# Kernel tuning notes

Measured on AMD Instinct MI355X. Metric: run time of the kernel, lower is better.

The kernel has to match this reference:

```python
import jax, jax.numpy as jnp
import numpy as np

HEADS = 8

def setup_inputs() -> dict:
    key = jax.random.key(0)
    ks = jax.random.split(key, 7)
    B, N, M, C = 4, 2048, 2048, 512
    s = 0.02
    return {
        "hidden_states": jax.random.normal(ks[0], (B, N, C), jnp.float32),
        "encoder_states": jax.random.normal(ks[1], (B, M, C), jnp.float32),
        "Wq": jax.random.normal(ks[2], (C, C), jnp.float32) * s,
        "Wk": jax.random.normal(ks[3], (C, C), jnp.float32) * s,
        "Wv": jax.random.normal(ks[4], (C, C), jnp.float32) * s,
        "Wo": jax.random.normal(ks[5], (C, C), jnp.float32) * s,
        "bo": jnp.zeros((C,), jnp.float32),
    }

def reference(hidden_states, encoder_states, Wq, Wk, Wv, Wo, bo):
    B, N, C = hidden_states.shape
    M = encoder_states.shape[1]
    H = HEADS
    dh = C // H
    scale = dh ** -0.5  # q.shape[-1] ** -0.5 in FlashAttentionFunction / attn.scale
    # projections (to_q/to_k/to_v, no bias as in diffusers CrossAttention)
    q = (hidden_states @ Wq).reshape(B, N, H, dh).transpose(0, 2, 1, 3)   # [B,H,N,dh]
    k = (encoder_states @ Wk).reshape(B, M, H, dh).transpose(0, 2, 1, 3)  # [B,H,M,dh]
    v = (encoder_states @ Wv).reshape(B, M, H, dh).transpose(0, 2, 1, 3)  # [B,H,M,dh]
    # baddbmm(scores) -> softmax -> bmm(values); no mask, non-causal
    scores = jnp.einsum('bhnd,bhmd->bhnm', q, k) * scale                  # [B,H,N,M]
    probs = jax.nn.softmax(scores, axis=-1)
    out = jnp.einsum('bhnm,bhmd->bhnd', probs, v)                         # [B,H,N,dh]
    out = out.transpose(0, 2, 1, 3).reshape(B, N, C)                      # batch_to_head_dim
    return out @ Wo + bo                                                  # to_out[0]; to_out[1] is dropout (identity at eval)
```

## Files before the change

### kernel.cpp

```cpp
#include <hip/hip_runtime.h>
#include <stdint.h>
#include <stddef.h>

typedef __bf16 bf16x8 __attribute__((ext_vector_type(8)));
typedef float f32x4 __attribute__((ext_vector_type(4)));
typedef float f32x16 __attribute__((ext_vector_type(16)));
typedef int int4v __attribute__((ext_vector_type(4)));
typedef unsigned short u16;
typedef unsigned int u32;

__device__ __forceinline__ u16 f2bf(float f) {
    union { float f; unsigned u; } x; x.f = f;
    unsigned r = x.u + 0x7fffu + ((x.u >> 16) & 1u);
    return (u16)(r >> 16);
}

__device__ __forceinline__ float fexp2(float x) { return __builtin_amdgcn_exp2f(x); }

__device__ __forceinline__ u32 cvtpk(float lo, float hi) {
    u32 r;
    asm("v_cvt_pk_bf16_f32 %0, %1, %2" : "=v"(r) : "v"(lo), "v"(hi));
    return r;
}

__device__ __forceinline__ void perm32swap(u32& a, u32& b) {
    asm("v_permlane32_swap_b32 %0, %1" : "+v"(a), "+v"(b));
}

__device__ __forceinline__ f32x16 mfma32(bf16x8 a, bf16x8 b, f32x16 c) {
    return __builtin_amdgcn_mfma_f32_32x32x16_bf16(a, b, c, 0, 0, 0);
}

__device__ __forceinline__ void gl16(const void* g, void* l) {
    __builtin_amdgcn_global_load_lds(
        (const __attribute__((address_space(1))) void*)g,
        (__attribute__((address_space(3))) void*)l, 16, 0, 0);
}

__global__ __launch_bounds__(256) void wtrans4(
        const float* __restrict__ Wq, const float* __restrict__ Wk,
        const float* __restrict__ Wv, const float* __restrict__ Wo,
        u16* __restrict__ oq, u16* __restrict__ ok,
        u16* __restrict__ ov, u16* __restrict__ oo) {
    const int z = blockIdx.z;
    const float* W = (z == 0) ? Wq : (z == 1) ? Wk : (z == 2) ? Wv : Wo;
    u16* O = (z == 0) ? oq : (z == 1) ? ok : (z == 2) ? ov : oo;
    int t  = blockIdx.x * 256 + threadIdx.x;
    int g  = t >> 12;
    int k0 = (t >> 9) & 7;
    int n  = t & 511;
    float v[8];
#pragma unroll
    for (int j = 0; j < 8; ++j)
        v[j] = W[(size_t)(k0 * 64 + g * 8 + j) * 512 + n];
    int gs = g ^ (n & 7);
    u16* dst = O + ((size_t)(k0 * 512 + n) * 8 + gs) * 8;
    ushort4 a, b;
    a.x = f2bf(v[0]); a.y = f2bf(v[1]); a.z = f2bf(v[2]); a.w = f2bf(v[3]);
    b.x = f2bf(v[4]); b.y = f2bf(v[5]); b.z = f2bf(v[6]); b.w = f2bf(v[7]);
    *(ushort4*)dst = a;
    *(ushort4*)(dst + 4) = b;
}

__global__ __launch_bounds__(256) void gemm_qkv(
        const float* __restrict__ hidden, const float* __restrict__ enc,
        const u16* __restrict__ wq, const u16* __restrict__ wk, const u16* __restrict__ wv,
        u16* __restrict__ qo, u16* __restrict__ ko, u16* __restrict__ vo) {
    __shared__ __align__(16) u16 As[128 * 64];
    __shared__ __align__(16) u16 Bs[128 * 64];
    const int z = blockIdx.z;
    const float* A = (z == 0) ? hidden : enc;
    const u16* Bp = (z == 0) ? wq : (z == 1) ? wk : wv;
    const int tid = threadIdx.x, lane = tid & 63, wave = tid >> 6;
    const int wr = (wave >> 1) * 64, wc = (wave & 1) * 64;
    const int brow = blockIdx.x * 128, bcol = blockIdx.y * 128;
    const int lrow = lane & 15;
    const int sr = tid >> 3, sc = tid & 7;

    f32x4 acc[4][4] = {};

    for (int k0s = 0; k0s < 8; ++k0s) {
        const u16* bsrc = Bp + ((size_t)(k0s * 512 + bcol) * 64) + (size_t)(wave * 256 + lane) * 8;
#pragma unroll
        for (int i = 0; i < 4; ++i)
            gl16(bsrc + i * 512, (char*)Bs + wave * 4096 + i * 1024);
#pragma unroll
        for (int i = 0; i < 4; ++i) {
            int r = i * 32 + sr;
            const float* src = A + (size_t)(brow + r) * 512 + k0s * 64 + sc * 8;
            float4 f0 = *(const float4*)src, f1 = *(const float4*)(src + 4);
            int4v w;
            w[0] = cvtpk(f0.x, f0.y); w[1] = cvtpk(f0.z, f0.w);
            w[2] = cvtpk(f1.x, f1.y); w[3] = cvtpk(f1.z, f1.w);
            *(int4v*)((char*)As + r * 128 + ((sc ^ (r & 7)) << 4)) = w;
        }
        __syncthreads();
#pragma unroll
        for (int kc = 0; kc < 2; ++kc) {
            const int kg = kc * 4 + (lane >> 4);
            bf16x8 af[4], bfr[4];
#pragma unroll
            for (int m = 0; m < 4; ++m) {
                int r = wr + m * 16 + lrow;
                af[m] = *(const bf16x8*)((char*)As + r * 128 + ((kg ^ (r & 7)) << 4));
            }
#pragma unroll
            for (int n = 0; n < 4; ++n) {
                int r = wc + n * 16 + lrow;
                bfr[n] = *(const bf16x8*)((char*)Bs + r * 128 + ((kg ^ (r & 7)) << 4));
            }
#pragma unroll
            for (int m = 0; m < 4; ++m)
#pragma unroll
                for (int n = 0; n < 4; ++n)
                    acc[m][n] = __builtin_amdgcn_mfma_f32_16x16x32_bf16(af[m], bfr[n], acc[m][n], 0, 0, 0);
        }
        __syncthreads();
    }

#pragma unroll
    for (int m = 0; m < 4; ++m) {
        int gr0 = brow + wr + m * 16 + ((lane >> 4) << 2);
#pragma unroll
        for (int n = 0; n < 4; ++n) {
            int gc = bcol + wc + n * 16 + lrow;
            int hh = gc >> 6, d = gc & 63;
            if (z == 2) {
                int b = gr0 >> 11, mm = gr0 & 2047;
                ushort4 pk;
                pk.x = f2bf(acc[m][n][0]); pk.y = f2bf(acc[m][n][1]);
                pk.z = f2bf(acc[m][n][2]); pk.w = f2bf(acc[m][n][3]);
                *(ushort4*)(vo + ((size_t)(b * 8 + hh) * 64 + d) * 2048 + mm) = pk;
            } else {
                u16* dst = (z == 0) ? qo : ko;
                const float s = (z == 0) ? 0.125f * 1.44269504f : 1.0f;
#pragma unroll
                for (int j = 0; j < 4; ++j) {
                    int gr = gr0 + j;
                    int b = gr >> 11, nn = gr & 2047;
                    dst[((size_t)(b * 8 + hh) * 2048 + nn) * 64 + d] = f2bf(acc[m][n][j] * s);
                }
            }
        }
    }
}

__global__ __launch_bounds__(256) void gemm_out(
        const u16* __restrict__ A, const u16* __restrict__ Bp,
        const float* __restrict__ bias, float* __restrict__ out) {
    __shared__ __align__(16) u16 As[128 * 64];
    __shared__ __align__(16) u16 Bs[64 * 64];
    const int tid = threadIdx.x, lane = tid & 63, wave = tid >> 6;
    const int wr = (wave >> 1) * 64, wc = (wave & 1) * 32;
    const int brow = blockIdx.x * 128, bcol = blockIdx.y * 64;
    const int lrow = lane & 15;
    const int ar = wave * 32 + (lane >> 3), ag = lane & 7;

    f32x4 acc[4][2] = {};

    for (int k0s = 0; k0s < 8; ++k0s) {
        const u16* asrc = A + (size_t)(brow + ar) * 512 + k0s * 64 + ag * 8;
#pragma unroll
        for (int i = 0; i < 4; ++i)
            gl16(asrc + (size_t)(i * 8) * 512, (char*)As + wave * 4096 + i * 1024);
        const u16* bsrc = Bp + ((size_t)(k0s * 512 + bcol) * 64) + (size_t)(wave * 128 + lane) * 8;
#pragma unroll
        for (int i = 0; i < 2; ++i)
            gl16(bsrc + i * 512, (char*)Bs + wave * 2048 + i * 1024);
        __syncthreads();
#pragma unroll
        for (int kc = 0; kc < 2; ++kc) {
            const int kg = kc * 4 + (lane >> 4);
            bf16x8 af[4], bfr[2];
#pragma unroll
            for (int m = 0; m < 4; ++m) {
                int r = wr + m * 16 + lrow;
                af[m] = *(const bf16x8*)((char*)As + r * 128 + ((kg ^ (r & 7)) << 4));
            }
#pragma unroll
            for (int n = 0; n < 2; ++n) {
                int r = wc + n * 16 + lrow;
                bfr[n] = *(const bf16x8*)((char*)Bs + r * 128 + ((kg ^ (r & 7)) << 4));
            }
#pragma unroll
            for (int m = 0; m < 4; ++m)
#pragma unroll
                for (int n = 0; n < 2; ++n)
                    acc[m][n] = __builtin_amdgcn_mfma_f32_16x16x32_bf16(af[m], bfr[n], acc[m][n], 0, 0, 0);
        }
        __syncthreads();
    }

#pragma unroll
    for (int m = 0; m < 4; ++m) {
        int gr0 = brow + wr + m * 16 + ((lane >> 4) << 2);
#pragma unroll
        for (int n = 0; n < 2; ++n) {
            int gc = bcol + wc + n * 16 + lrow;
            float bv = bias[gc];
#pragma unroll
            for (int j = 0; j < 4; ++j)
                out[(size_t)(gr0 + j) * 512 + gc] = acc[m][n][j] + bv;
        }
    }
}

__global__ __launch_bounds__(1024, 4) void flash_attn(
        const u16* __restrict__ Q, const u16* __restrict__ K,
        const u16* __restrict__ VT, u16* __restrict__ Oa) {
    __shared__ __align__(16) char smem[65536];

    const int tid  = threadIdx.x;
    const int lane = tid & 63;
    const int wave = tid >> 6;
    const int qgrp = wave >> 2;
    const int qtr  = wave & 3;
    const int ql   = lane & 31;
    const int hl   = lane >> 5;
    const int bid  = blockIdx.x;
    const int lid  = (bid & 7) * 64 + (bid >> 3);
    const int bh   = lid >> 4;
    const int qt   = lid & 15;
    const int qg   = qt * 128 + qgrp * 32 + ql;

    const u16* qp = Q + ((size_t)bh * 2048 + qg) * 64 + 8 * hl;
    bf16x8 qf[4];
#pragma unroll
    for (int kc = 0; kc < 4; ++kc) qf[kc] = *(const bf16x8*)(qp + 16 * kc);

    const bool isK = wave < 8;
    const int sq   = isK ? (wave >> 1) : ((wave - 8) >> 1);
    const int i0   = (wave & 1) * 2;
    const int loK = (lane >> 3) * 64 + (((lane & 7) ^ ((lane >> 3) & 7)) * 8);
    const int loV = (lane >> 2) * 2048 + (((lane & 3) ^ ((lane >> 3) & 3)) * 8);
    const u16* gsrc0 = isK
        ? K  + ((size_t)bh * 2048 + sq * 512 + i0 * 8) * 64 + loK
        : VT + (size_t)bh * 131072 + (size_t)(i0 * 16) * 2048 + sq * 512 + loV;
    char* ldst0 = smem + (isK ? 0 : 16384) + sq * 4096 + i0 * 1024;

#define STAGE(b, t) do { \
    const u16* s0_ = gsrc0 + (isK ? (size_t)(t) * 2048 : (size_t)(t) * 32); \
    char* d0_ = ldst0 + (b) * 32768; \
    gl16(s0_, d0_); \
    gl16(s0_ + (isK ? 512 : 32768), d0_ + 1024); \
} while (0)

    f32x16 acc0 = {}, acc1 = {};
    float ls0 = 0.f, ls1 = 0.f, ls2 = 0.f, ls3 = 0.f;

    STAGE(0, 0);
    __syncthreads();

    for (int t = 0; t < 16; ++t) {
        const int b = t & 1;
        if (t < 15) STAGE(b ^ 1, t + 1);

        const char* Kt = smem + b * 32768 + qtr * 4096;
        const char* Vt = smem + b * 32768 + 16384 + qtr * 4096;

        f32x16 st = {};
        __builtin_amdgcn_s_setprio(1);
#pragma unroll
        for (int kc = 0; kc < 4; ++kc) {
            bf16x8 kf = *(const bf16x8*)(Kt + ql * 128 + (((kc * 2 + hl) ^ (ql & 7)) << 4));
            st = mfma32(kf, qf[kc], st);
        }
        __builtin_amdgcn_s_setprio(0);

#pragma unroll
        for (int r = 0; r < 16; r += 4) {
            st[r]   = fexp2(st[r]);   ls0 += st[r];
            st[r+1] = fexp2(st[r+1]); ls1 += st[r+1];
            st[r+2] = fexp2(st[r+2]); ls2 += st[r+2];
            st[r+3] = fexp2(st[r+3]); ls3 += st[r+3];
        }

        __builtin_amdgcn_s_setprio(1);
#pragma unroll
        for (int kc = 0; kc < 2; ++kc) {
            u32 P0 = cvtpk(st[8 * kc + 0], st[8 * kc + 1]);
            u32 P1 = cvtpk(st[8 * kc + 2], st[8 * kc + 3]);
            u32 Q0 = cvtpk(st[8 * kc + 4], st[8 * kc + 5]);
            u32 Q1 = cvtpk(st[8 * kc + 6], st[8 * kc + 7]);
            perm32swap(P0, Q0);
            perm32swap(P1, Q1);
            union { bf16x8 v; u32 u[4]; } bb;
            bb.u[0] = P0; bb.u[1] = P1; bb.u[2] = Q0; bb.u[3] = Q1;
            const int sg = ((kc * 2 + hl) ^ ((ql >> 1) & 3)) << 4;
            bf16x8 v0 = *(const bf16x8*)(Vt + ql * 64 + sg);
            bf16x8 v1 = *(const bf16x8*)(Vt + (32 + ql) * 64 + sg);
            acc0 = mfma32(v0, bb.v, acc0);
            acc1 = mfma32(v1, bb.v, acc1);
        }
        __builtin_amdgcn_s_setprio(0);

        __syncthreads();
    }
#undef STAGE

    float lsum = (ls0 + ls1) + (ls2 + ls3);
    lsum += __shfl_xor(lsum, 32);

    float* CB = (float*)smem;
    float* LS = (float*)(smem + 32768);
    for (int p = 1; p < 4; ++p) {
        if (qtr == p) {
            float* R = CB + qgrp * 2048;
#pragma unroll
            for (int j = 0; j < 4; ++j)
                *(f32x4*)(R + lane * 32 + ((j ^ (lane & 7)) << 2)) =
                    f32x4{acc0[4*j], acc0[4*j+1], acc0[4*j+2], acc0[4*j+3]};
#pragma unroll
            for (int j = 0; j < 4; ++j)
                *(f32x4*)(R + lane * 32 + (((j + 4) ^ (lane & 7)) << 2)) =
                    f32x4{acc1[4*j], acc1[4*j+1], acc1[4*j+2], acc1[4*j+3]};
            LS[qgrp * 64 + lane] = lsum;
        }
        __syncthreads();
        if (qtr == 0) {
            float* R = CB + qgrp * 2048;
#pragma unroll
            for (int j = 0; j < 4; ++j) {
                f32x4 v = *(const f32x4*)(R + lane * 32 + ((j ^ (lane & 7)) << 2));
                acc0[4*j] += v[0]; acc0[4*j+1] += v[1]; acc0[4*j+2] += v[2]; acc0[4*j+3] += v[3];
            }
#pragma unroll
            for (int j = 0; j < 4; ++j) {
                f32x4 v = *(const f32x4*)(R + lane * 32 + (((j + 4) ^ (lane & 7)) << 2));
                acc1[4*j] += v[0]; acc1[4*j+1] += v[1]; acc1[4*j+2] += v[2]; acc1[4*j+3] += v[3];
            }
            lsum += LS[qgrp * 64 + lane];
        }
        __syncthreads();
    }

    if (qtr == 0) {
        float inv = 1.0f / lsum;
        int b_ = bh >> 3, hd = bh & 7;
        u16* orow = Oa + ((size_t)b_ * 2048 + qg) * 512 + hd * 64;
#pragma unroll
        for (int db = 0; db < 2; ++db) {
            const f32x16 a = db ? acc1 : acc0;
#pragma unroll
            for (int rg = 0; rg < 4; ++rg) {
                int d0 = (((db * 4 + rg) ^ (qg & 7)) << 3) + hl * 4;
                ushort4 pk;
                pk.x = f2bf(a[rg * 4 + 0] * inv);
                pk.y = f2bf(a[rg * 4 + 1] * inv);
                pk.z = f2bf(a[rg * 4 + 2] * inv);
                pk.w = f2bf(a[rg * 4 + 3] * inv);
                *(ushort4*)(orow + d0) = pk;
            }
        }
    }
}

extern "C" void kernel_launch(void* const* d_in, const int* in_sizes, int n_in,
                              void* d_out, int out_size, void* d_ws, size_t ws_size,
                              hipStream_t stream) {
    const float* hidden = (const float*)d_in[0];
    const float* enc    = (const float*)d_in[1];
    const float* Wq     = (const float*)d_in[2];
    const float* Wk     = (const float*)d_in[3];
    const float* Wv     = (const float*)d_in[4];
    const float* Wo     = (const float*)d_in[5];
    const float* bo     = (const float*)d_in[6];
    float* out = (float*)d_out;

    char* ws = (char*)d_ws;
    const size_t MB = 1ull << 20;
    u16* q_bf  = (u16*)(ws + 0 * MB);
    u16* k_bf  = (u16*)(ws + 8 * MB);
    u16* vt_bf = (u16*)(ws + 16 * MB);
    u16* at_bf = (u16*)(ws + 24 * MB);
    u16* wq_t  = (u16*)(ws + 32 * MB);
    u16* wk_t  = (u16*)(ws + 32 * MB + 512 * 1024);
    u16* wv_t  = (u16*)(ws + 33 * MB);
    u16* wo_t  = (u16*)(ws + 33 * MB + 512 * 1024);

    dim3 wg(128, 1, 4);
    wtrans4<<<wg, 256, 0, stream>>>(Wq, Wk, Wv, Wo, wq_t, wk_t, wv_t, wo_t);

    dim3 qkvg(64, 4, 3);
    gemm_qkv<<<qkvg, 256, 0, stream>>>(hidden, enc, wq_t, wk_t, wv_t, q_bf, k_bf, vt_bf);

    flash_attn<<<512, 1024, 0, stream>>>(q_bf, k_bf, vt_bf, at_bf);

    dim3 og(64, 8);
    gemm_out<<<og, 256, 0, stream>>>(at_bf, wo_t, bo, out);
}
```

Measured before the change: 95.34 us.

## Pre-swizzle K/V into MFMA fragment layout and load directly from global to registers

The QKV projection now writes K and V in the exact per-lane MFMA fragment order. This lets the attention kernel load them straight from global memory into registers, with double-buffered register prefetch, instead of staging them through LDS with barriers every tile. The attention block shrinks from 1024 to 256 threads. Each wave now handles two 32-row query groups and half of the key range, and the two halves are combined through LDS at the end. This removes LDS traffic and per-tile barriers, at the cost of more registers and no LDS sharing of K/V between waves, so the same data is fetched more times from global memory or L2.

```diff
diff --git a/kernel.cpp b/kernel.cpp
--- a/kernel.cpp
+++ b/kernel.cpp
@@ -124,22 +124,35 @@
 #pragma unroll
         for (int n = 0; n < 4; ++n) {
             int gc = bcol + wc + n * 16 + lrow;
-            int hh = gc >> 6, d = gc & 63;
-            if (z == 2) {
-                int b = gr0 >> 11, mm = gr0 & 2047;
+            int hh2 = gc >> 6, d = gc & 63;
+            int b = gr0 >> 11;
+            int bh2 = b * 8 + hh2;
+            if (z == 0) {
+                int nn = gr0 & 2047;
+#pragma unroll
+                for (int j = 0; j < 4; ++j)
+                    qo[((size_t)bh2 * 2048 + nn + j) * 64 + d] =
+                        f2bf(acc[m][n][j] * (0.125f * 1.44269504f));
+            } else if (z == 1) {
+                int kc = d >> 4, e = d & 7, dl = (d >> 3) & 1;
+#pragma unroll
+                for (int j = 0; j < 4; ++j) {
+                    int nn = (gr0 & 2047) + j;
+                    size_t off = ((((size_t)bh2 * 32 + (nn >> 6)) * 2 + ((nn >> 5) & 1)) * 4 + kc) * 512
+                               + (size_t)((nn & 31) + dl * 32) * 8 + e;
+                    ko[off] = f2bf(acc[m][n][j]);
+                }
+            } else {
+                int nn0 = gr0 & 2047;
+                int t = nn0 >> 6, jj = (nn0 >> 4) & 3;
+                int db = d >> 5;
+                int lfr = (d & 31) + ((nn0 >> 3) & 1) * 32;
+                int e0 = nn0 & 7;
+                size_t off = ((((size_t)bh2 * 32 + t) * 4 + jj) * 2 + db) * 512 + (size_t)lfr * 8 + e0;
                 ushort4 pk;
                 pk.x = f2bf(acc[m][n][0]); pk.y = f2bf(acc[m][n][1]);
                 pk.z = f2bf(acc[m][n][2]); pk.w = f2bf(acc[m][n][3]);
-                *(ushort4*)(vo + ((size_t)(b * 8 + hh) * 64 + d) * 2048 + mm) = pk;
-            } else {
-                u16* dst = (z == 0) ? qo : ko;
-                const float s = (z == 0) ? 0.125f * 1.44269504f : 1.0f;
-#pragma unroll
-                for (int j = 0; j < 4; ++j) {
-                    int gr = gr0 + j;
-                    int b = gr >> 11, nn = gr & 2047;
-                    dst[((size_t)(b * 8 + hh) * 2048 + nn) * 64 + d] = f2bf(acc[m][n][j] * s);
-                }
+                *(ushort4*)(vo + off) = pk;
             }
         }
     }
@@ -205,154 +218,154 @@
     }
 }
 
-__global__ __launch_bounds__(1024, 4) void flash_attn(
-        const u16* __restrict__ Q, const u16* __restrict__ K,
-        const u16* __restrict__ VT, u16* __restrict__ Oa) {
-    __shared__ __align__(16) char smem[65536];
+__global__ __launch_bounds__(256) void flash_attn(
+        const u16* __restrict__ Q, const u16* __restrict__ KF,
+        const u16* __restrict__ VF, u16* __restrict__ Oa) {
+    __shared__ __align__(16) float CB[2][64 * 64];
+    __shared__ float LSH[2][64];
 
     const int tid  = threadIdx.x;
     const int lane = tid & 63;
-    const int wave = tid >> 6;
-    const int qgrp = wave >> 2;
-    const int qtr  = wave & 3;
+    const int wid  = tid >> 6;
     const int ql   = lane & 31;
     const int hl   = lane >> 5;
+    const int pid  = wid >> 1;
+    const int half = wid & 1;
     const int bid  = blockIdx.x;
     const int lid  = (bid & 7) * 64 + (bid >> 3);
     const int bh   = lid >> 4;
-    const int qt   = lid & 15;
-    const int qg   = qt * 128 + qgrp * 32 + ql;
-
-    const u16* qp = Q + ((size_t)bh * 2048 + qg) * 64 + 8 * hl;
-    bf16x8 qf[4];
-#pragma unroll
-    for (int kc = 0; kc < 4; ++kc) qf[kc] = *(const bf16x8*)(qp + 16 * kc);
-
-    const bool isK = wave < 8;
-    const int sq   = isK ? (wave >> 1) : ((wave - 8) >> 1);
-    const int i0   = (wave & 1) * 2;
-    const int loK = (lane >> 3) * 64 + (((lane & 7) ^ ((lane >> 3) & 7)) * 8);
-    const int loV = (lane >> 2) * 2048 + (((lane & 3) ^ ((lane >> 3) & 3)) * 8);
-    const u16* gsrc0 = isK
-        ? K  + ((size_t)bh * 2048 + sq * 512 + i0 * 8) * 64 + loK
-        : VT + (size_t)bh * 131072 + (size_t)(i0 * 16) * 2048 + sq * 512 + loV;
-    char* ldst0 = smem + (isK ? 0 : 16384) + sq * 4096 + i0 * 1024;
-
-#define STAGE(b, t) do { \
-    const u16* s0_ = gsrc0 + (isK ? (size_t)(t) * 2048 : (size_t)(t) * 32); \
-    char* d0_ = ldst0 + (b) * 32768; \
-    gl16(s0_, d0_); \
-    gl16(s0_ + (isK ? 512 : 32768), d0_ + 1024); \
+    const int qt   = (lid & 15) * 2 + pid;
+    const int qbase = qt * 64;
+
+    bf16x8 qf[2][4];
+#pragma unroll
+    for (int qg = 0; qg < 2; ++qg)
+#pragma unroll
+        for (int kc = 0; kc < 4; ++kc)
+            qf[qg][kc] = *(const bf16x8*)(Q + ((size_t)bh * 2048 + qbase + qg * 32 + ql) * 64 + kc * 16 + hl * 8);
+
+    const u16* kb = KF + (size_t)bh * 131072 + (size_t)(half * 32) * 2048 + lane * 8;
+    const u16* vb = VF + (size_t)bh * 131072 + (size_t)(half * 32) * 2048 + lane * 8;
+
+    f32x16 acc00 = {}, acc01 = {}, acc10 = {}, acc11 = {};
+    float ls[2][4] = {};
+
+    bf16x8 kA[4], vA[4], kB[4], vB[4];
+
+#define LOADHS(KB_, VB_, s) do { \
+    _Pragma("unroll") \
+    for (int kc = 0; kc < 4; ++kc) KB_[kc] = *(const bf16x8*)(kb + (s) * 2048 + kc * 512); \
+    _Pragma("unroll") \
+    for (int f = 0; f < 4; ++f)  VB_[f] = *(const bf16x8*)(vb + (s) * 2048 + f * 512); \
 } while (0)
 
-    f32x16 acc0 = {}, acc1 = {};
-    float ls0 = 0.f, ls1 = 0.f, ls2 = 0.f, ls3 = 0.f;
-
-    STAGE(0, 0);
+#define COMPQG(STN, AC0, AC1, qgi, KB_, VB_) do { \
+    f32x16 STN = {}; \
+    __builtin_amdgcn_s_setprio(1); \
+    _Pragma("unroll") \
+    for (int kc = 0; kc < 4; ++kc) STN = mfma32(KB_[kc], qf[qgi][kc], STN); \
+    __builtin_amdgcn_s_setprio(0); \
+    _Pragma("unroll") \
+    for (int r = 0; r < 16; r += 4) { \
+        STN[r]   = fexp2(STN[r]);   ls[qgi][0] += STN[r]; \
+        STN[r+1] = fexp2(STN[r+1]); ls[qgi][1] += STN[r+1]; \
+        STN[r+2] = fexp2(STN[r+2]); ls[qgi][2] += STN[r+2]; \
+        STN[r+3] = fexp2(STN[r+3]); ls[qgi][3] += STN[r+3]; \
+    } \
+    __builtin_amdgcn_s_setprio(1); \
+    _Pragma("unroll") \
+    for (int jl = 0; jl < 2; ++jl) { \
+        u32 A0 = cvtpk(STN[8*jl+0], STN[8*jl+1]); \
+        u32 A1 = cvtpk(STN[8*jl+2], STN[8*jl+3]); \
+        u32 B0 = cvtpk(STN[8*jl+4], STN[8*jl+5]); \
+        u32 B1 = cvtpk(STN[8*jl+6], STN[8*jl+7]); \
+        perm32swap(A0, B0); \
+        perm32swap(A1, B1); \
+        union { bf16x8 v; u32 u[4]; } bb; \
+        bb.u[0] = A0; bb.u[1] = A1; bb.u[2] = B0; bb.u[3] = B1; \
+        AC0 = mfma32(VB_[jl*2+0], bb.v, AC0); \
+        AC1 = mfma32(VB_[jl*2+1], bb.v, AC1); \
+    } \
+    __builtin_amdgcn_s_setprio(0); \
+} while (0)
+
+    LOADHS(kA, vA, 0);
+    LOADHS(kB, vB, 1);
+    for (int s = 0; s < 32; s += 2) {
+        COMPQG(stA0, acc00, acc01, 0, kA, vA);
+        COMPQG(stA1, acc10, acc11, 1, kA, vA);
+        if (s + 2 < 32) LOADHS(kA, vA, s + 2);
+        COMPQG(stB0, acc00, acc01, 0, kB, vB);
+        COMPQG(stB1, acc10, acc11, 1, kB, vB);
+        if (s + 3 < 32) LOADHS(kB, vB, s + 3);
+    }
+#undef LOADHS
+#undef COMPQG
+
+    float lsum0 = (ls[0][0] + ls[0][1]) + (ls[0][2] + ls[0][3]);
+    float lsum1 = (ls[1][0] + ls[1][1]) + (ls[1][2] + ls[1][3]);
+    lsum0 += __shfl_xor(lsum0, 32);
+    lsum1 += __shfl_xor(lsum1, 32);
+
+#define PUB(qgi, A0, A1, LSV) do { \
+    int qlc = (qgi) * 32 + ql; \
+    _Pragma("unroll") \
+    for (int rg = 0; rg < 4; ++rg) { \
+        int g0 = (rg * 2 + hl) ^ (qlc & 15); \
+        *(f32x4*)&CB[pid][qlc * 64 + g0 * 4] = f32x4{A0[4*rg], A0[4*rg+1], A0[4*rg+2], A0[4*rg+3]}; \
+        int g1 = (8 + rg * 2 + hl) ^ (qlc & 15); \
+        *(f32x4*)&CB[pid][qlc * 64 + g1 * 4] = f32x4{A1[4*rg], A1[4*rg+1], A1[4*rg+2], A1[4*rg+3]}; \
+    } \
+    if (hl == 0) LSH[pid][qlc] = LSV; \
+} while (0)
+
+#define RED(qgi, A0, A1, LSV) do { \
+    int qlc = (qgi) * 32 + ql; \
+    _Pragma("unroll") \
+    for (int rg = 0; rg < 4; ++rg) { \
+        int g0 = (rg * 2 + hl) ^ (qlc & 15); \
+        f32x4 v0 = *(const f32x4*)&CB[pid][qlc * 64 + g0 * 4]; \
+        A0[4*rg] += v0[0]; A0[4*rg+1] += v0[1]; A0[4*rg+2] += v0[2]; A0[4*rg+3] += v0[3]; \
+        int g1 = (8 + rg * 2 + hl) ^ (qlc & 15); \
+        f32x4 v1 = *(const f32x4*)&CB[pid][qlc * 64 + g1 * 4]; \
+        A1[4*rg] += v1[0]; A1[4*rg+1] += v1[1]; A1[4*rg+2] += v1[2]; A1[4*rg+3] += v1[3]; \
+    } \
+    LSV += LSH[pid][qlc]; \
+} while (0)
+
+    if (half == 1) {
+        PUB(0, acc00, acc01, lsum0);
+        PUB(1, acc10, acc11, lsum1);
+    }
     __syncthreads();
-
-    for (int t = 0; t < 16; ++t) {
-        const int b = t & 1;
-        if (t < 15) STAGE(b ^ 1, t + 1);
-
-        const char* Kt = smem + b * 32768 + qtr * 4096;
-        const char* Vt = smem + b * 32768 + 16384 + qtr * 4096;
-
-        f32x16 st = {};
-        __builtin_amdgcn_s_setprio(1);
-#pragma unroll
-        for (int kc = 0; kc < 4; ++kc) {
-            bf16x8 kf = *(const bf16x8*)(Kt + ql * 128 + (((kc * 2 + hl) ^ (ql & 7)) << 4));
-            st = mfma32(kf, qf[kc], st);
-        }
-        __builtin_amdgcn_s_setprio(0);
-
-#pragma unroll
-        for (int r = 0; r < 16; r += 4) {
-            st[r]   = fexp2(st[r]);   ls0 += st[r];
-            st[r+1] = fexp2(st[r+1]); ls1 += st[r+1];
-            st[r+2] = fexp2(st[r+2]); ls2 += st[r+2];
-            st[r+3] = fexp2(st[r+3]); ls3 += st[r+3];
-        }
-
-        __builtin_amdgcn_s_setprio(1);
-#pragma unroll
-        for (int kc = 0; kc < 2; ++kc) {
-            u32 P0 = cvtpk(st[8 * kc + 0], st[8 * kc + 1]);
-            u32 P1 = cvtpk(st[8 * kc + 2], st[8 * kc + 3]);
-            u32 Q0 = cvtpk(st[8 * kc + 4], st[8 * kc + 5]);
-            u32 Q1 = cvtpk(st[8 * kc + 6], st[8 * kc + 7]);
-            perm32swap(P0, Q0);
-            perm32swap(P1, Q1);
-            union { bf16x8 v; u32 u[4]; } bb;
-            bb.u[0] = P0; bb.u[1] = P1; bb.u[2] = Q0; bb.u[3] = Q1;
-            const int sg = ((kc * 2 + hl) ^ ((ql >> 1) & 3)) << 4;
-            bf16x8 v0 = *(const bf16x8*)(Vt + ql * 64 + sg);
-            bf16x8 v1 = *(const bf16x8*)(Vt + (32 + ql) * 64 + sg);
-            acc0 = mfma32(v0, bb.v, acc0);
-            acc1 = mfma32(v1, bb.v, acc1);
-        }
-        __builtin_amdgcn_s_setprio(0);
-
-        __syncthreads();
-    }
-#undef STAGE
-
-    float lsum = (ls0 + ls1) + (ls2 + ls3);
-    lsum += __shfl_xor(lsum, 32);
-
-    float* CB = (float*)smem;
-    float* LS = (float*)(smem + 32768);
-    for (int p = 1; p < 4; ++p) {
-        if (qtr == p) {
-            float* R = CB + qgrp * 2048;
-#pragma unroll
-            for (int j = 0; j < 4; ++j)
-                *(f32x4*)(R + lane * 32 + ((j ^ (lane & 7)) << 2)) =
-                    f32x4{acc0[4*j], acc0[4*j+1], acc0[4*j+2], acc0[4*j+3]};
-#pragma unroll
-            for (int j = 0; j < 4; ++j)
-                *(f32x4*)(R + lane * 32 + (((j + 4) ^ (lane & 7)) << 2)) =
-                    f32x4{acc1[4*j], acc1[4*j+1], acc1[4*j+2], acc1[4*j+3]};
-            LS[qgrp * 64 + lane] = lsum;
-        }
-        __syncthreads();
-        if (qtr == 0) {
-            float* R = CB + qgrp * 2048;
-#pragma unroll
-            for (int j = 0; j < 4; ++j) {
-                f32x4 v = *(const f32x4*)(R + lane * 32 + ((j ^ (lane & 7)) << 2));
-                acc0[4*j] += v[0]; acc0[4*j+1] += v[1]; acc0[4*j+2] += v[2]; acc0[4*j+3] += v[3];
-            }
-#pragma unroll
-            for (int j = 0; j < 4; ++j) {
-                f32x4 v = *(const f32x4*)(R + lane * 32 + (((j + 4) ^ (lane & 7)) << 2));
-                acc1[4*j] += v[0]; acc1[4*j+1] += v[1]; acc1[4*j+2] += v[2]; acc1[4*j+3] += v[3];
-            }
-            lsum += LS[qgrp * 64 + lane];
-        }
-        __syncthreads();
-    }
-
-    if (qtr == 0) {
-        float inv = 1.0f / lsum;
+    if (half == 0) {
+        RED(0, acc00, acc01, lsum0);
+        RED(1, acc10, acc11, lsum1);
+        float inv0 = 1.0f / lsum0, inv1 = 1.0f / lsum1;
         int b_ = bh >> 3, hd = bh & 7;
-        u16* orow = Oa + ((size_t)b_ * 2048 + qg) * 512 + hd * 64;
-#pragma unroll
-        for (int db = 0; db < 2; ++db) {
-            const f32x16 a = db ? acc1 : acc0;
-#pragma unroll
-            for (int rg = 0; rg < 4; ++rg) {
-                int d0 = (((db * 4 + rg) ^ (qg & 7)) << 3) + hl * 4;
-                ushort4 pk;
-                pk.x = f2bf(a[rg * 4 + 0] * inv);
-                pk.y = f2bf(a[rg * 4 + 1] * inv);
-                pk.z = f2bf(a[rg * 4 + 2] * inv);
-                pk.w = f2bf(a[rg * 4 + 3] * inv);
-                *(ushort4*)(orow + d0) = pk;
-            }
-        }
-    }
+#define STO(qgi, A0, A1, INV) do { \
+        int qrow = qbase + (qgi) * 32 + ql; \
+        u16* orow = Oa + ((size_t)b_ * 2048 + qrow) * 512 + hd * 64; \
+        _Pragma("unroll") \
+        for (int rg = 0; rg < 4; ++rg) { \
+            int d00 = ((rg ^ (qrow & 7)) << 3) + hl * 4; \
+            ushort4 p0; \
+            p0.x = f2bf(A0[4*rg] * INV);   p0.y = f2bf(A0[4*rg+1] * INV); \
+            p0.z = f2bf(A0[4*rg+2] * INV); p0.w = f2bf(A0[4*rg+3] * INV); \
+            *(ushort4*)(orow + d00) = p0; \
+            int d01 = (((4 + rg) ^ (qrow & 7)) << 3) + hl * 4; \
+            ushort4 p1; \
+            p1.x = f2bf(A1[4*rg] * INV);   p1.y = f2bf(A1[4*rg+1] * INV); \
+            p1.z = f2bf(A1[4*rg+2] * INV); p1.w = f2bf(A1[4*rg+3] * INV); \
+            *(ushort4*)(orow + d01) = p1; \
+        } \
+} while (0)
+        STO(0, acc00, acc01, inv0);
+        STO(1, acc10, acc11, inv1);
+#undef STO
+    }
+#undef PUB
+#undef RED
 }
 
 extern "C" void kernel_launch(void* const* d_in, const int* in_sizes, int n_in,
@@ -370,8 +383,8 @@
     char* ws = (char*)d_ws;
     const size_t MB = 1ull << 20;
     u16* q_bf  = (u16*)(ws + 0 * MB);
-    u16* k_bf  = (u16*)(ws + 8 * MB);
-    u16* vt_bf = (u16*)(ws + 16 * MB);
+    u16* kf_bf = (u16*)(ws + 8 * MB);
+    u16* vf_bf = (u16*)(ws + 16 * MB);
     u16* at_bf = (u16*)(ws + 24 * MB);
     u16* wq_t  = (u16*)(ws + 32 * MB);
     u16* wk_t  = (u16*)(ws + 32 * MB + 512 * 1024);
@@ -382,9 +395,9 @@
     wtrans4<<<wg, 256, 0, stream>>>(Wq, Wk, Wv, Wo, wq_t, wk_t, wv_t, wo_t);
 
     dim3 qkvg(64, 4, 3);
-    gemm_qkv<<<qkvg, 256, 0, stream>>>(hidden, enc, wq_t, wk_t, wv_t, q_bf, k_bf, vt_bf);
-
-    flash_attn<<<512, 1024, 0, stream>>>(q_bf, k_bf, vt_bf, at_bf);
+    gemm_qkv<<<qkvg, 256, 0, stream>>>(hidden, enc, wq_t, wk_t, wv_t, q_bf, kf_bf, vf_bf);
+
+    flash_attn<<<512, 256, 0, stream>>>(q_bf, kf_bf, vf_bf, at_bf);
 
     dim3 og(64, 8);
     gemm_out<<<og, 256, 0, stream>>>(at_bf, wo_t, bo, out);
```

Result: slower. 101.5 us (+6.5%).

## Shrink flash-attention blocks to 4 waves, each computing two query subtiles

Applied to the files above, without the earlier changes.

The attention kernel moves from 16 waves per 1024-thread block to 4 waves per 256-thread block. Each wave now handles 64 queries (two 32-row subtiles) against half of each key tile, so every K and V fragment read from shared memory feeds two MFMAs. Staging is split so one wave pair loads K and the other loads V, and the cross-wave reduction collapses to a single publish/reduce step between the two halves. This cuts LDS traffic and synchronisation per FLOP, at the cost of more registers per wave and fewer waves to hide latency.

```diff
diff --git a/kernel.cpp b/kernel.cpp
--- a/kernel.cpp
+++ b/kernel.cpp
@@ -205,7 +205,7 @@
     }
 }
 
-__global__ __launch_bounds__(1024, 4) void flash_attn(
+__global__ __launch_bounds__(256, 2) void flash_attn(
         const u16* __restrict__ Q, const u16* __restrict__ K,
         const u16* __restrict__ VT, u16* __restrict__ Oa) {
     __shared__ __align__(16) char smem[65536];
@@ -213,40 +213,46 @@
     const int tid  = threadIdx.x;
     const int lane = tid & 63;
     const int wave = tid >> 6;
-    const int qgrp = wave >> 2;
-    const int qtr  = wave & 3;
+    const int qg   = wave >> 1;
+    const int half = wave & 1;
     const int ql   = lane & 31;
     const int hl   = lane >> 5;
     const int bid  = blockIdx.x;
     const int lid  = (bid & 7) * 64 + (bid >> 3);
     const int bh   = lid >> 4;
     const int qt   = lid & 15;
-    const int qg   = qt * 128 + qgrp * 32 + ql;
-
-    const u16* qp = Q + ((size_t)bh * 2048 + qg) * 64 + 8 * hl;
-    bf16x8 qf[4];
-#pragma unroll
-    for (int kc = 0; kc < 4; ++kc) qf[kc] = *(const bf16x8*)(qp + 16 * kc);
-
-    const bool isK = wave < 8;
-    const int sq   = isK ? (wave >> 1) : ((wave - 8) >> 1);
-    const int i0   = (wave & 1) * 2;
-    const int loK = (lane >> 3) * 64 + (((lane & 7) ^ ((lane >> 3) & 7)) * 8);
-    const int loV = (lane >> 2) * 2048 + (((lane & 3) ^ ((lane >> 3) & 3)) * 8);
-    const u16* gsrc0 = isK
-        ? K  + ((size_t)bh * 2048 + sq * 512 + i0 * 8) * 64 + loK
-        : VT + (size_t)bh * 131072 + (size_t)(i0 * 16) * 2048 + sq * 512 + loV;
-    char* ldst0 = smem + (isK ? 0 : 16384) + sq * 4096 + i0 * 1024;
-
-#define STAGE(b, t) do { \
-    const u16* s0_ = gsrc0 + (isK ? (size_t)(t) * 2048 : (size_t)(t) * 32); \
-    char* d0_ = ldst0 + (b) * 32768; \
-    gl16(s0_, d0_); \
-    gl16(s0_ + (isK ? 512 : 32768), d0_ + 1024); \
+    const int qbase = qt * 128 + qg * 64;
+
+    bf16x8 qf[2][4];
+#pragma unroll
+    for (int sq = 0; sq < 2; ++sq)
+#pragma unroll
+        for (int kc = 0; kc < 4; ++kc)
+            qf[sq][kc] = *(const bf16x8*)(Q + ((size_t)bh * 2048 + qbase + sq * 32 + ql) * 64 + kc * 16 + hl * 8);
+
+    const int srow = lane >> 3;
+    const int sgr  = (lane & 7) ^ srow;
+    const u16* ksrc = K  + (size_t)bh * 131072 + (size_t)(half * 1024 + srow) * 64 + sgr * 8;
+    const u16* vsrc = VT + (size_t)bh * 131072 + (size_t)srow * 2048 + half * 1024 + sgr * 8;
+    char* kdst = smem + half * 8192;
+    char* vdst = smem + 16384 + half * 8192;
+
+#define STAGE(b_, t_) do { \
+    if (qg == 0) { \
+        const u16* s_ = ksrc + (size_t)(t_) * 4096; \
+        char* d_ = kdst + (b_) * 32768; \
+        _Pragma("unroll") \
+        for (int i = 0; i < 8; ++i) gl16(s_ + i * 512, d_ + i * 1024); \
+    } else { \
+        const u16* s_ = vsrc + (t_) * 64; \
+        char* d_ = vdst + (b_) * 32768; \
+        _Pragma("unroll") \
+        for (int i = 0; i < 8; ++i) gl16(s_ + (size_t)i * 16384, d_ + i * 1024); \
+    } \
 } while (0)
 
-    f32x16 acc0 = {}, acc1 = {};
-    float ls0 = 0.f, ls1 = 0.f, ls2 = 0.f, ls3 = 0.f;
+    f32x16 acc00 = {}, acc01 = {}, acc10 = {}, acc11 = {};
+    float ls[2][4] = {};
 
     STAGE(0, 0);
     __syncthreads();
@@ -254,105 +260,146 @@
     for (int t = 0; t < 16; ++t) {
         const int b = t & 1;
         if (t < 15) STAGE(b ^ 1, t + 1);
-
-        const char* Kt = smem + b * 32768 + qtr * 4096;
-        const char* Vt = smem + b * 32768 + 16384 + qtr * 4096;
-
-        f32x16 st = {};
-        __builtin_amdgcn_s_setprio(1);
-#pragma unroll
-        for (int kc = 0; kc < 4; ++kc) {
-            bf16x8 kf = *(const bf16x8*)(Kt + ql * 128 + (((kc * 2 + hl) ^ (ql & 7)) << 4));
-            st = mfma32(kf, qf[kc], st);
-        }
-        __builtin_amdgcn_s_setprio(0);
-
-#pragma unroll
-        for (int r = 0; r < 16; r += 4) {
-            st[r]   = fexp2(st[r]);   ls0 += st[r];
-            st[r+1] = fexp2(st[r+1]); ls1 += st[r+1];
-            st[r+2] = fexp2(st[r+2]); ls2 += st[r+2];
-            st[r+3] = fexp2(st[r+3]); ls3 += st[r+3];
-        }
-
-        __builtin_amdgcn_s_setprio(1);
-#pragma unroll
-        for (int kc = 0; kc < 2; ++kc) {
-            u32 P0 = cvtpk(st[8 * kc + 0], st[8 * kc + 1]);
-            u32 P1 = cvtpk(st[8 * kc + 2], st[8 * kc + 3]);
-            u32 Q0 = cvtpk(st[8 * kc + 4], st[8 * kc + 5]);
-            u32 Q1 = cvtpk(st[8 * kc + 6], st[8 * kc + 7]);
-            perm32swap(P0, Q0);
-            perm32swap(P1, Q1);
-            union { bf16x8 v; u32 u[4]; } bb;
-            bb.u[0] = P0; bb.u[1] = P1; bb.u[2] = Q0; bb.u[3] = Q1;
-            const int sg = ((kc * 2 + hl) ^ ((ql >> 1) & 3)) << 4;
-            bf16x8 v0 = *(const bf16x8*)(Vt + ql * 64 + sg);
-            bf16x8 v1 = *(const bf16x8*)(Vt + (32 + ql) * 64 + sg);
-            acc0 = mfma32(v0, bb.v, acc0);
-            acc1 = mfma32(v1, bb.v, acc1);
-        }
-        __builtin_amdgcn_s_setprio(0);
-
+        const char* Kt = smem + b * 32768 + half * 8192;
+        const char* Vt = smem + b * 32768 + 16384 + half * 8192;
+
+#pragma unroll
+        for (int ks = 0; ks < 2; ++ks) {
+            bf16x8 kf[4];
+#pragma unroll
+            for (int kc = 0; kc < 4; ++kc) {
+                int kr = ks * 32 + ql;
+                kf[kc] = *(const bf16x8*)(Kt + kr * 128 + (((kc * 2 + hl) ^ (kr & 7)) << 4));
+            }
+            bf16x8 vf[2][2];
+#pragma unroll
+            for (int jl = 0; jl < 2; ++jl)
+#pragma unroll
+                for (int dh2 = 0; dh2 < 2; ++dh2) {
+                    int dr = dh2 * 32 + ql;
+                    vf[jl][dh2] = *(const bf16x8*)(Vt + dr * 128 + (((ks * 4 + jl * 2 + hl) ^ (dr & 7)) << 4));
+                }
+
+            f32x16 st0 = {}, st1 = {};
+            __builtin_amdgcn_s_setprio(1);
+#pragma unroll
+            for (int kc = 0; kc < 4; ++kc) {
+                st0 = mfma32(kf[kc], qf[0][kc], st0);
+                st1 = mfma32(kf[kc], qf[1][kc], st1);
+            }
+            __builtin_amdgcn_s_setprio(0);
+
+#pragma unroll
+            for (int r = 0; r < 16; r += 4) {
+                st0[r]   = fexp2(st0[r]);   ls[0][0] += st0[r];
+                st0[r+1] = fexp2(st0[r+1]); ls[0][1] += st0[r+1];
+                st0[r+2] = fexp2(st0[r+2]); ls[0][2] += st0[r+2];
+                st0[r+3] = fexp2(st0[r+3]); ls[0][3] += st0[r+3];
+                st1[r]   = fexp2(st1[r]);   ls[1][0] += st1[r];
+                st1[r+1] = fexp2(st1[r+1]); ls[1][1] += st1[r+1];
+                st1[r+2] = fexp2(st1[r+2]); ls[1][2] += st1[r+2];
+                st1[r+3] = fexp2(st1[r+3]); ls[1][3] += st1[r+3];
+            }
+
+            __builtin_amdgcn_s_setprio(1);
+#pragma unroll
+            for (int jl = 0; jl < 2; ++jl) {
+                u32 A0 = cvtpk(st0[8*jl+0], st0[8*jl+1]);
+                u32 A1 = cvtpk(st0[8*jl+2], st0[8*jl+3]);
+                u32 B0 = cvtpk(st0[8*jl+4], st0[8*jl+5]);
+                u32 B1 = cvtpk(st0[8*jl+6], st0[8*jl+7]);
+                perm32swap(A0, B0);
+                perm32swap(A1, B1);
+                union { bf16x8 v; u32 u[4]; } bb0;
+                bb0.u[0] = A0; bb0.u[1] = A1; bb0.u[2] = B0; bb0.u[3] = B1;
+                acc00 = mfma32(vf[jl][0], bb0.v, acc00);
+                acc01 = mfma32(vf[jl][1], bb0.v, acc01);
+                u32 C0 = cvtpk(st1[8*jl+0], st1[8*jl+1]);
+                u32 C1 = cvtpk(st1[8*jl+2], st1[8*jl+3]);
+                u32 D0 = cvtpk(st1[8*jl+4], st1[8*jl+5]);
+                u32 D1 = cvtpk(st1[8*jl+6], st1[8*jl+7]);
+                perm32swap(C0, D0);
+                perm32swap(C1, D1);
+                union { bf16x8 v; u32 u[4]; } bb1;
+                bb1.u[0] = C0; bb1.u[1] = C1; bb1.u[2] = D0; bb1.u[3] = D1;
+                acc10 = mfma32(vf[jl][0], bb1.v, acc10);
+                acc11 = mfma32(vf[jl][1], bb1.v, acc11);
+            }
+            __builtin_amdgcn_s_setprio(0);
+        }
         __syncthreads();
     }
 #undef STAGE
 
-    float lsum = (ls0 + ls1) + (ls2 + ls3);
-    lsum += __shfl_xor(lsum, 32);
+    float lsum0 = (ls[0][0] + ls[0][1]) + (ls[0][2] + ls[0][3]);
+    float lsum1 = (ls[1][0] + ls[1][1]) + (ls[1][2] + ls[1][3]);
+    lsum0 += __shfl_xor(lsum0, 32);
+    lsum1 += __shfl_xor(lsum1, 32);
 
     float* CB = (float*)smem;
     float* LS = (float*)(smem + 32768);
-    for (int p = 1; p < 4; ++p) {
-        if (qtr == p) {
-            float* R = CB + qgrp * 2048;
-#pragma unroll
-            for (int j = 0; j < 4; ++j)
-                *(f32x4*)(R + lane * 32 + ((j ^ (lane & 7)) << 2)) =
-                    f32x4{acc0[4*j], acc0[4*j+1], acc0[4*j+2], acc0[4*j+3]};
-#pragma unroll
-            for (int j = 0; j < 4; ++j)
-                *(f32x4*)(R + lane * 32 + (((j + 4) ^ (lane & 7)) << 2)) =
-                    f32x4{acc1[4*j], acc1[4*j+1], acc1[4*j+2], acc1[4*j+3]};
-            LS[qgrp * 64 + lane] = lsum;
-        }
-        __syncthreads();
-        if (qtr == 0) {
-            float* R = CB + qgrp * 2048;
-#pragma unroll
-            for (int j = 0; j < 4; ++j) {
-                f32x4 v = *(const f32x4*)(R + lane * 32 + ((j ^ (lane & 7)) << 2));
-                acc0[4*j] += v[0]; acc0[4*j+1] += v[1]; acc0[4*j+2] += v[2]; acc0[4*j+3] += v[3];
-            }
-#pragma unroll
-            for (int j = 0; j < 4; ++j) {
-                f32x4 v = *(const f32x4*)(R + lane * 32 + (((j + 4) ^ (lane & 7)) << 2));
-                acc1[4*j] += v[0]; acc1[4*j+1] += v[1]; acc1[4*j+2] += v[2]; acc1[4*j+3] += v[3];
-            }
-            lsum += LS[qgrp * 64 + lane];
-        }
-        __syncthreads();
-    }
-
-    if (qtr == 0) {
-        float inv = 1.0f / lsum;
+
+#define PUBQ(sq, A0, A1, LSV) do { \
+    int qq = (sq) * 32 + ql; \
+    float* R = CB + qg * 4096 + qq * 64; \
+    _Pragma("unroll") \
+    for (int rg = 0; rg < 4; ++rg) { \
+        int g0 = (2 * rg + hl) ^ (qq & 15); \
+        *(f32x4*)(R + g0 * 4) = f32x4{A0[4*rg], A0[4*rg+1], A0[4*rg+2], A0[4*rg+3]}; \
+        int g1 = (8 + 2 * rg + hl) ^ (qq & 15); \
+        *(f32x4*)(R + g1 * 4) = f32x4{A1[4*rg], A1[4*rg+1], A1[4*rg+2], A1[4*rg+3]}; \
+    } \
+    if (hl == 0) LS[qg * 64 + qq] = LSV; \
+} while (0)
+
+#define REDQ(sq, A0, A1, LSV) do { \
+    int qq = (sq) * 32 + ql; \
+    const float* R = CB + qg * 4096 + qq * 64; \
+    _Pragma("unroll") \
+    for (int rg = 0; rg < 4; ++rg) { \
+        int g0 = (2 * rg + hl) ^ (qq & 15); \
+        f32x4 v0 = *(const f32x4*)(R + g0 * 4); \
+        A0[4*rg] += v0[0]; A0[4*rg+1] += v0[1]; A0[4*rg+2] += v0[2]; A0[4*rg+3] += v0[3]; \
+        int g1 = (8 + 2 * rg + hl) ^ (qq & 15); \
+        f32x4 v1 = *(const f32x4*)(R + g1 * 4); \
+        A1[4*rg] += v1[0]; A1[4*rg+1] += v1[1]; A1[4*rg+2] += v1[2]; A1[4*rg+3] += v1[3]; \
+    } \
+    LSV += LS[qg * 64 + qq]; \
+} while (0)
+
+    if (half == 1) {
+        PUBQ(0, acc00, acc01, lsum0);
+        PUBQ(1, acc10, acc11, lsum1);
+    }
+    __syncthreads();
+    if (half == 0) {
+        REDQ(0, acc00, acc01, lsum0);
+        REDQ(1, acc10, acc11, lsum1);
+        float inv0 = 1.0f / lsum0, inv1 = 1.0f / lsum1;
         int b_ = bh >> 3, hd = bh & 7;
-        u16* orow = Oa + ((size_t)b_ * 2048 + qg) * 512 + hd * 64;
-#pragma unroll
-        for (int db = 0; db < 2; ++db) {
-            const f32x16 a = db ? acc1 : acc0;
-#pragma unroll
-            for (int rg = 0; rg < 4; ++rg) {
-                int d0 = (((db * 4 + rg) ^ (qg & 7)) << 3) + hl * 4;
-                ushort4 pk;
-                pk.x = f2bf(a[rg * 4 + 0] * inv);
-                pk.y = f2bf(a[rg * 4 + 1] * inv);
-                pk.z = f2bf(a[rg * 4 + 2] * inv);
-                pk.w = f2bf(a[rg * 4 + 3] * inv);
-                *(ushort4*)(orow + d0) = pk;
-            }
-        }
-    }
+#define STOQ(sq, A0, A1, INV) do { \
+        int qrow = qbase + (sq) * 32 + ql; \
+        u16* orow = Oa + ((size_t)b_ * 2048 + qrow) * 512 + hd * 64; \
+        _Pragma("unroll") \
+        for (int rg = 0; rg < 4; ++rg) { \
+            int d00 = ((rg ^ (qrow & 7)) << 3) + hl * 4; \
+            ushort4 p0; \
+            p0.x = f2bf(A0[4*rg] * INV);   p0.y = f2bf(A0[4*rg+1] * INV); \
+            p0.z = f2bf(A0[4*rg+2] * INV); p0.w = f2bf(A0[4*rg+3] * INV); \
+            *(ushort4*)(orow + d00) = p0; \
+            int d01 = (((4 + rg) ^ (qrow & 7)) << 3) + hl * 4; \
+            ushort4 p1; \
+            p1.x = f2bf(A1[4*rg] * INV);   p1.y = f2bf(A1[4*rg+1] * INV); \
+            p1.z = f2bf(A1[4*rg+2] * INV); p1.w = f2bf(A1[4*rg+3] * INV); \
+            *(ushort4*)(orow + d01) = p1; \
+        } \
+} while (0)
+        STOQ(0, acc00, acc01, inv0);
+        STOQ(1, acc10, acc11, inv1);
+#undef STOQ
+    }
+#undef PUBQ
+#undef REDQ
 }
 
 extern "C" void kernel_launch(void* const* d_in, const int* in_sizes, int n_in,
@@ -384,7 +431,7 @@
     dim3 qkvg(64, 4, 3);
     gemm_qkv<<<qkvg, 256, 0, stream>>>(hidden, enc, wq_t, wk_t, wv_t, q_bf, k_bf, vt_bf);
 
-    flash_attn<<<512, 1024, 0, stream>>>(q_bf, k_bf, vt_bf, at_bf);
+    flash_attn<<<512, 256, 0, stream>>>(q_bf, k_bf, vt_bf, at_bf);
 
     dim3 og(64, 8);
     gemm_out<<<og, 256, 0, stream>>>(at_bf, wo_t, bo, out);
```

Measured after the change: 87.72 us. 8.0% less time.
